# Kernel tuning notes

Hardware: AMD Instinct MI355X
Metric: run time of the kernel (lower is better)

Reference implementation:

```python
import jax, jax.numpy as jnp
import numpy as np

TAU = 0.2
LW = 0.5
EPS = 1e-12  # tf.math.l2_normalize epsilon


def _l2norm(x):
    ss = jnp.sum(x * x, axis=-1, keepdims=True)
    return x * jax.lax.rsqrt(jnp.maximum(ss, EPS))


def _global_head(f, W1, b1, W2, b2):
    g = jnp.mean(f, axis=(1, 2))            # GlobalAveragePooling2D -> [B, C]
    h = jax.nn.relu(g @ W1 + b1)
    return h @ W2 + b2                      # [B, 128]


def _dense_head(f, W1, b1, W2, b2):
    # 1x1 convs == per-pixel matmuls
    h = jax.nn.relu(jnp.einsum('bhwc,cd->bhwd', f, W1) + b1)
    return jnp.einsum('bhwd,de->bhwe', h, W2) + b2  # [B, H, W, 128]


def _info_nce(q, k):
    logits = (q @ k.T) / TAU                # [N, N]
    lse = jax.nn.logsumexp(logits, axis=-1)
    pos = jnp.diagonal(logits)
    return jnp.mean(lse - pos)


def setup_inputs() -> dict:
    key = jax.random.key(0)
    ks = jax.random.split(key, 10)
    B, H, W, C = 128, 7, 7, 2048
    Dh, De = 2048, 128
    s1 = 1.0 / np.sqrt(C)
    s2 = 1.0 / np.sqrt(Dh)
    inp = {
        'feat_q': jax.random.normal(ks[0], (B, H, W, C), jnp.float32),
        'feat_k': jax.random.normal(ks[1], (B, H, W, C), jnp.float32),
        'Wg1': jax.random.normal(ks[2], (C, Dh), jnp.float32) * s1,
        'bg1': jnp.zeros((Dh,), jnp.float32),
        'Wg2': jax.random.normal(ks[3], (Dh, De), jnp.float32) * s2,
        'bg2': jnp.zeros((De,), jnp.float32),
        'Wd1': jax.random.normal(ks[4], (C, Dh), jnp.float32) * s1,
        'bd1': jnp.zeros((Dh,), jnp.float32),
        'Wd2': jax.random.normal(ks[5], (Dh, De), jnp.float32) * s2,
        'bd2': jnp.zeros((De,), jnp.float32),
        'mWg1': jax.random.normal(ks[6], (C, Dh), jnp.float32) * s1,
        'mbg1': jnp.zeros((Dh,), jnp.float32),
        'mWg2': jax.random.normal(ks[7], (Dh, De), jnp.float32) * s2,
        'mbg2': jnp.zeros((De,), jnp.float32),
        'mWd1': jax.random.normal(ks[8], (C, Dh), jnp.float32) * s1,
        'mbd1': jnp.zeros((Dh,), jnp.float32),
        'mWd2': jax.random.normal(ks[9], (Dh, De), jnp.float32) * s2,
        'mbd2': jnp.zeros((De,), jnp.float32),
    }
    return inp


def reference(feat_q, feat_k, Wg1, bg1, Wg2, bg2, Wd1, bd1, Wd2, bd2,
              mWg1, mbg1, mWg2, mbg2, mWd1, mbd1, mWd2, mbd2):
    # query (student) branch
    q_g = _l2norm(_global_head(feat_q, Wg1, bg1, Wg2, bg2))      # [B, 128]
    q_d = _l2norm(_dense_head(feat_q, Wd1, bd1, Wd2, bd2))       # [B, H, W, 128]
    # key (momentum teacher) branch, stop-gradient as in train_step
    k_g = jax.lax.stop_gradient(_l2norm(_global_head(feat_k, mWg1, mbg1, mWg2, mbg2)))
    k_d = jax.lax.stop_gradient(_l2norm(_dense_head(feat_k, mWd1, mbd1, mWd2, mbd2)))

    l_g = _info_nce(q_g, k_g)

    B, H, W, De = q_d.shape
    f1 = q_d.reshape(B, H * W, De)
    f2 = k_d.reshape(B, H * W, De)
    sim = jnp.einsum('bnc,bmc->bnm', f1, f2)                     # [B, HW, HW]
    idx = jnp.argmax(sim, axis=-1)                               # [B, HW]
    matched = jnp.take_along_axis(f2, idx[..., None], axis=1)    # [B, HW, 128]

    l_d = _info_nce(f1.reshape(-1, De), matched.reshape(-1, De))
    total = (1.0 - LW) * l_g + LW * l_d
    return total
```

## Files before the change

kernel.cpp:

```cpp
#include <hip/hip_runtime.h>
#include <cstddef>

typedef __bf16 bf16x8 __attribute__((ext_vector_type(8)));
typedef float  f32x4  __attribute__((ext_vector_type(4)));
typedef unsigned short u16x8 __attribute__((ext_vector_type(8)));

__device__ __forceinline__ float b2f(unsigned short u) {
    union { unsigned int i; float f; } v; v.i = ((unsigned int)u) << 16; return v.f;
}
__device__ __forceinline__ unsigned short f2b(float f) {
    union { float f; unsigned int i; } v; v.f = f;
    unsigned int r = v.i + 0x7fffu + ((v.i >> 16) & 1u);
    return (unsigned short)(r >> 16);
}
__device__ __forceinline__ void gl_lds16(const void* g, void* l) {
    __builtin_amdgcn_global_load_lds((const __attribute__((address_space(1))) void*)g,
                                     (__attribute__((address_space(3))) void*)l,
                                     16, 0, 0);
}

__global__ __launch_bounds__(64) void detect_kernel(const unsigned short* __restrict__ feat,
                                                    int* __restrict__ flag) {
    __shared__ int cnt;
    if (threadIdx.x == 0) cnt = 0;
    __syncthreads();
    int c = 0;
    for (int i = threadIdx.x; i < 256; i += 64) {
        float v = b2f(feat[i]);
        if (fabsf(v) > 100.0f) ++c;
    }
    atomicAdd(&cnt, c);
    __syncthreads();
    if (threadIdx.x == 0) *flag = (cnt > 16) ? 1 : 0;
}

__global__ __launch_bounds__(256) void zero_kernel(float* __restrict__ p, int n4) {
    int i = blockIdx.x * 256 + threadIdx.x;
    const f32x4 z = {0.f, 0.f, 0.f, 0.f};
    if (i < n4) ((f32x4*)p)[i] = z;
}

__global__ __launch_bounds__(256) void pool_kernel(const void* __restrict__ fq,
                                                   const void* __restrict__ fk,
                                                   unsigned short* __restrict__ gq,
                                                   unsigned short* __restrict__ gk,
                                                   const int* __restrict__ flagp) {
    int fl = *flagp;
    int c = blockIdx.x * 256 + threadIdx.x;
    int b = blockIdx.y;
    const void* src = blockIdx.z ? fk : fq;
    unsigned short* dst = blockIdx.z ? gk : gq;
    size_t base = (size_t)b * 49 * 2048 + c;
    float s = 0.f;
    if (fl) {
        const float* sf = (const float*)src;
        #pragma unroll
        for (int p = 0; p < 49; ++p) s += sf[base + (size_t)p * 2048];
    } else {
        const unsigned short* su = (const unsigned short*)src;
        #pragma unroll
        for (int p = 0; p < 49; ++p) s += b2f(su[base + (size_t)p * 2048]);
    }
    dst[(size_t)b * 2048 + c] = f2b(s * (1.0f / 49.0f));
}

__global__ __launch_bounds__(256) void transpose4_kernel(
    const void* __restrict__ s0, const void* __restrict__ s1,
    const void* __restrict__ s2, const void* __restrict__ s3,
    unsigned short* __restrict__ d0, unsigned short* __restrict__ d1,
    unsigned short* __restrict__ d2, unsigned short* __restrict__ d3,
    int rows, int cols, const int* __restrict__ flagp) {
    int fl = *flagp;
    int z = blockIdx.z;
    const void* in = (z == 0) ? s0 : (z == 1) ? s1 : (z == 2) ? s2 : s3;
    unsigned short* out = (z == 0) ? d0 : (z == 1) ? d1 : (z == 2) ? d2 : d3;
    __shared__ unsigned short tile[32][33];
    int bx = blockIdx.x * 32, by = blockIdx.y * 32;
    int tx = threadIdx.x & 31, ty = threadIdx.x >> 5;
    if (fl) {
        const float* inf = (const float*)in;
        #pragma unroll
        for (int i = 0; i < 32; i += 8)
            tile[ty + i][tx] = f2b(inf[(size_t)(by + ty + i) * cols + (bx + tx)]);
    } else {
        const unsigned short* inu = (const unsigned short*)in;
        #pragma unroll
        for (int i = 0; i < 32; i += 8)
            tile[ty + i][tx] = inu[(size_t)(by + ty + i) * cols + (bx + tx)];
    }
    __syncthreads();
    #pragma unroll
    for (int i = 0; i < 32; i += 8)
        out[(size_t)(bx + ty + i) * rows + (by + tx)] = tile[tx][ty + i];
}

__global__ __launch_bounds__(256) void mlp_kernel(
    const void* __restrict__ Aq, const void* __restrict__ Ak,
    const unsigned short* __restrict__ gq, const unsigned short* __restrict__ gk,
    const unsigned short* __restrict__ BTdq, const unsigned short* __restrict__ BTdk,
    const unsigned short* __restrict__ BTgq, const unsigned short* __restrict__ BTgk,
    const unsigned short* __restrict__ W2dq, const unsigned short* __restrict__ W2dk,
    const unsigned short* __restrict__ W2gq, const unsigned short* __restrict__ W2gk,
    const void* __restrict__ b1dq, const void* __restrict__ b1dk,
    const void* __restrict__ b1gq, const void* __restrict__ b1gk,
    float* __restrict__ outdq, float* __restrict__ outdk,
    float* __restrict__ outgq, float* __restrict__ outgk,
    const int* __restrict__ flagp)
{
    int fl = *flagp;
    int z  = blockIdx.z;
    int isg = (blockIdx.y == 49);
    const void* A; const unsigned short* Bt; const unsigned short* W2;
    const void* b1; float* outp;
    if (!isg) {
        A = z ? Ak : Aq;  Bt = z ? BTdk : BTdq;  W2 = z ? W2dk : W2dq;
        b1 = z ? b1dk : b1dq;  outp = z ? outdk : outdq;
    } else {
        A = z ? (const void*)gk : (const void*)gq;  Bt = z ? BTgk : BTgq;
        W2 = z ? W2gk : W2gq;  b1 = z ? b1gk : b1gq;  outp = z ? outgk : outgq;
    }
    int af32 = (!isg) && fl;
    const int K = 2048;

    __shared__ unsigned short As[128 * 64];
    __shared__ unsigned short Bs[128 * 64];
    __shared__ unsigned short Hs[128 * 72];

    int tid  = threadIdx.x;
    int lane = tid & 63;
    int w    = tid >> 6;
    int wm = w & 1, wn = w >> 1;
    int quad = lane >> 4, l16 = lane & 15;
    size_t m0 = isg ? 0 : (size_t)blockIdx.y * 128;
    size_t n0 = (size_t)blockIdx.x * 128;

    int lrow = lane >> 3;
    int kc   = (lane & 7) ^ lrow;

    const unsigned short* gA[4];
    const unsigned short* gB[4];
    unsigned short* lA[4];
    unsigned short* lB[4];
    if (!af32) {
        const unsigned short* Au = (const unsigned short*)A;
        #pragma unroll
        for (int c = 0; c < 4; ++c) {
            int row = w * 32 + c * 8 + lrow;
            gA[c] = Au + (m0 + row) * (size_t)K + kc * 8;
            lA[c] = As + w * 2048 + c * 512;
        }
    }
    #pragma unroll
    for (int c = 0; c < 4; ++c) {
        int row = w * 32 + c * 8 + lrow;
        gB[c] = Bt + (n0 + row) * (size_t)K + kc * 8;
        lB[c] = Bs + w * 2048 + c * 512;
    }

    const f32x4 zero4 = {0.f, 0.f, 0.f, 0.f};
    f32x4 acc[4][4];
    #pragma unroll
    for (int i = 0; i < 4; ++i)
        #pragma unroll
        for (int j = 0; j < 4; ++j) acc[i][j] = zero4;

    int swz = l16 & 7;
    for (int kb = 0; kb < K / 64; ++kb) {
        __syncthreads();
        if (af32) {
            const float* Af = (const float*)A;
            #pragma unroll
            for (int i = 0; i < 4; ++i) {
                int l = tid + 256 * i;
                int row = l >> 3, kcp = l & 7;
                int kcg = kcp ^ (row & 7);
                size_t gidx = (m0 + row) * (size_t)K + kb * 64 + kcg * 8;
                f32x4 v0 = *(const f32x4*)(Af + gidx);
                f32x4 v1 = *(const f32x4*)(Af + gidx + 4);
                u16x8 o;
                o[0]=f2b(v0[0]); o[1]=f2b(v0[1]); o[2]=f2b(v0[2]); o[3]=f2b(v0[3]);
                o[4]=f2b(v1[0]); o[5]=f2b(v1[1]); o[6]=f2b(v1[2]); o[7]=f2b(v1[3]);
                *(u16x8*)(As + row * 64 + kcp * 8) = o;
            }
        } else {
            #pragma unroll
            for (int c = 0; c < 4; ++c) { gl_lds16(gA[c], lA[c]); gA[c] += 64; }
        }
        #pragma unroll
        for (int c = 0; c < 4; ++c) { gl_lds16(gB[c], lB[c]); gB[c] += 64; }
        __syncthreads();
        #pragma unroll
        for (int k0 = 0; k0 < 64; k0 += 32) {
            bf16x8 af[4], bfr[4];
            #pragma unroll
            for (int mt = 0; mt < 4; ++mt) {
                int row = wm * 64 + mt * 16 + l16;
                int sc  = (((k0 >> 3) + quad) ^ swz) << 3;
                af[mt] = *(const bf16x8*)(As + row * 64 + sc);
            }
            #pragma unroll
            for (int nt = 0; nt < 4; ++nt) {
                int row = wn * 64 + nt * 16 + l16;
                int sc  = (((k0 >> 3) + quad) ^ swz) << 3;
                bfr[nt] = *(const bf16x8*)(Bs + row * 64 + sc);
            }
            #pragma unroll
            for (int mt = 0; mt < 4; ++mt)
                #pragma unroll
                for (int nt = 0; nt < 4; ++nt)
                    acc[mt][nt] = __builtin_amdgcn_mfma_f32_16x16x32_bf16(af[mt], bfr[nt], acc[mt][nt], 0, 0, 0);
        }
    }

    float b1v[4];
    #pragma unroll
    for (int nt = 0; nt < 4; ++nt) {
        int col = (int)n0 + wn * 64 + nt * 16 + l16;
        b1v[nt] = fl ? ((const float*)b1)[col] : b2f(((const unsigned short*)b1)[col]);
    }

    f32x4 acc2[4][4];
    #pragma unroll
    for (int i = 0; i < 4; ++i)
        #pragma unroll
        for (int j = 0; j < 4; ++j) acc2[i][j] = zero4;

    #pragma unroll
    for (int hf = 0; hf < 2; ++hf) {
        __syncthreads();
        if (wn == hf) {
            #pragma unroll
            for (int mt = 0; mt < 4; ++mt)
                #pragma unroll
                for (int nt = 0; nt < 4; ++nt)
                    #pragma unroll
                    for (int r = 0; r < 4; ++r) {
                        float v = fmaxf(acc[mt][nt][r] + b1v[nt], 0.f);
                        Hs[(wm * 64 + mt * 16 + quad * 4 + r) * 72 + nt * 16 + l16] = f2b(v);
                    }
        } else {
            #pragma unroll
            for (int c = 0; c < 8; ++c) {
                const unsigned short* g = W2 + (size_t)(wm * 64 + c * 8 + lrow) * 2048
                                          + n0 + hf * 64 + kc * 8;
                gl_lds16(g, As + wm * 4096 + c * 512);
            }
        }
        __syncthreads();
        #pragma unroll
        for (int k0 = 0; k0 < 64; k0 += 32) {
            bf16x8 ha[4], wb[4];
            #pragma unroll
            for (int mt = 0; mt < 4; ++mt)
                ha[mt] = *(const bf16x8*)(Hs + (wm * 64 + mt * 16 + l16) * 72 + k0 + quad * 8);
            #pragma unroll
            for (int et = 0; et < 4; ++et) {
                int row = wn * 64 + et * 16 + l16;
                int sc  = (((k0 >> 3) + quad) ^ swz) << 3;
                wb[et] = *(const bf16x8*)(As + row * 64 + sc);
            }
            #pragma unroll
            for (int mt = 0; mt < 4; ++mt)
                #pragma unroll
                for (int et = 0; et < 4; ++et)
                    acc2[mt][et] = __builtin_amdgcn_mfma_f32_16x16x32_bf16(ha[mt], wb[et], acc2[mt][et], 0, 0, 0);
        }
    }

    #pragma unroll
    for (int et = 0; et < 4; ++et) {
        int col = wn * 64 + et * 16 + l16;
        #pragma unroll
        for (int mt = 0; mt < 4; ++mt)
            #pragma unroll
            for (int r = 0; r < 4; ++r) {
                size_t row = m0 + wm * 64 + mt * 16 + quad * 4 + r;
                atomicAdd(&outp[row * 128 + col], acc2[mt][et][r]);
            }
    }
}

__global__ __launch_bounds__(128) void l2norm_all_kernel(
    const float* __restrict__ rawdq, const float* __restrict__ rawdk,
    const float* __restrict__ rawgq, const float* __restrict__ rawgk,
    const void* __restrict__ bd2, const void* __restrict__ mbd2,
    const void* __restrict__ bg2, const void* __restrict__ mbg2,
    unsigned short* __restrict__ qd, unsigned short* __restrict__ kd,
    unsigned short* __restrict__ qg, unsigned short* __restrict__ kg,
    const int* __restrict__ flagp) {
    int fl = *flagp;
    int b = blockIdx.x;
    const float* in; const void* bias; unsigned short* out; int r;
    if (b < 6272)       { in = rawdq; bias = bd2;  out = qd; r = b; }
    else if (b < 12544) { in = rawdk; bias = mbd2; out = kd; r = b - 6272; }
    else if (b < 12672) { in = rawgq; bias = bg2;  out = qg; r = b - 12544; }
    else                { in = rawgk; bias = mbg2; out = kg; r = b - 12672; }
    int t = threadIdx.x;
    float bv = fl ? ((const float*)bias)[t] : b2f(((const unsigned short*)bias)[t]);
    float x = in[(size_t)r * 128 + t] + bv;
    float s = x * x;
    #pragma unroll
    for (int off = 32; off >= 1; off >>= 1) s += __shfl_xor(s, off);
    __shared__ float ws2[2];
    if ((t & 63) == 0) ws2[t >> 6] = s;
    __syncthreads();
    float tot = ws2[0] + ws2[1];
    float rs = rsqrtf(fmaxf(tot, 1e-12f));
    out[(size_t)r * 128 + t] = f2b(x * rs);
}

__global__ __launch_bounds__(256) void simmatch_kernel(const unsigned short* __restrict__ qd,
                                                       const unsigned short* __restrict__ kd,
                                                       unsigned short* __restrict__ matched,
                                                       float* __restrict__ pos) {
    __shared__ float f1s[49 * 128];
    __shared__ float f2s[49 * 128];
    int b = blockIdx.x;
    int t = threadIdx.x;
    size_t base = (size_t)b * 49 * 128;
    for (int i = t; i < 49 * 128; i += 256) {
        f1s[i] = b2f(qd[base + i]);
        f2s[i] = b2f(kd[base + i]);
    }
    __syncthreads();
    int i = t >> 2, q4 = t & 3;
    if (i < 49) {
        int mlo = q4 * 13;
        int mhi = mlo + 13; if (mhi > 49) mhi = 49;
        float best = -1e30f; int bi = 1 << 20;
        const f32x4* va = (const f32x4*)(f1s + i * 128);
        for (int m = mlo; m < mhi; ++m) {
            const f32x4* vb = (const f32x4*)(f2s + m * 128);
            float d = 0.f;
            #pragma unroll
            for (int j = 0; j < 32; ++j) {
                f32x4 a = va[j], bb = vb[j];
                d += a[0]*bb[0] + a[1]*bb[1] + a[2]*bb[2] + a[3]*bb[3];
            }
            if (d > best) { best = d; bi = m; }
        }
        #pragma unroll
        for (int off = 1; off < 4; off <<= 1) {
            float ov = __shfl_xor(best, off);
            int   oi = __shfl_xor(bi, off);
            if (ov > best || (ov == best && oi < bi)) { best = ov; bi = oi; }
        }
        if (q4 == 0) pos[b * 49 + i] = best * 5.0f;
        for (int j = q4 * 32; j < q4 * 32 + 32; ++j)
            matched[base + (size_t)i * 128 + j] = f2b(f2s[bi * 128 + j]);
    }
}

#define KS 136
__global__ __launch_bounds__(256) void lse_kernel(const unsigned short* __restrict__ qd,
                                                  const unsigned short* __restrict__ matched,
                                                  float* __restrict__ lsep) {
    __shared__ unsigned short As[128 * KS];
    __shared__ unsigned short Bs[64 * KS];
    __shared__ float rsum[128];
    int tid  = threadIdx.x;
    int lane = tid & 63, wave = tid >> 6;
    int wm = wave & 1, wn = wave >> 1;
    int quad = lane >> 4, l16 = lane & 15;
    size_t m0 = (size_t)blockIdx.x * 128;
    int z = blockIdx.y;

    #pragma unroll
    for (int i = 0; i < 8; ++i) {
        int l = tid + 256 * i;
        int row = l >> 4, ko = (l & 15) << 3;
        u16x8 v = *(const u16x8*)(qd + (m0 + row) * 128 + ko);
        *(u16x8*)(As + row * KS + ko) = v;
    }
    if (tid < 128) rsum[tid] = 0.f;

    float rs[4][4];
    #pragma unroll
    for (int mt = 0; mt < 4; ++mt)
        #pragma unroll
        for (int r = 0; r < 4; ++r) rs[mt][r] = 0.f;

    const f32x4 zero4 = {0.f, 0.f, 0.f, 0.f};
    int nlo = z * 896, nhi = nlo + 896;
    for (int n0 = nlo; n0 < nhi; n0 += 64) {
        __syncthreads();
        #pragma unroll
        for (int i = 0; i < 4; ++i) {
            int l = tid + 256 * i;
            int row = l >> 4, ko = (l & 15) << 3;
            u16x8 v = *(const u16x8*)(matched + (size_t)(n0 + row) * 128 + ko);
            *(u16x8*)(Bs + row * KS + ko) = v;
        }
        __syncthreads();
        f32x4 acc[4][2];
        #pragma unroll
        for (int mt = 0; mt < 4; ++mt) { acc[mt][0] = zero4; acc[mt][1] = zero4; }
        #pragma unroll
        for (int k0 = 0; k0 < 128; k0 += 32) {
            bf16x8 af[4], bfr[2];
            #pragma unroll
            for (int mt = 0; mt < 4; ++mt)
                af[mt] = *(const bf16x8*)(As + (wm * 64 + mt * 16 + l16) * KS + k0 + quad * 8);
            #pragma unroll
            for (int nt = 0; nt < 2; ++nt)
                bfr[nt] = *(const bf16x8*)(Bs + (wn * 32 + nt * 16 + l16) * KS + k0 + quad * 8);
            #pragma unroll
            for (int mt = 0; mt < 4; ++mt)
                #pragma unroll
                for (int nt = 0; nt < 2; ++nt)
                    acc[mt][nt] = __builtin_amdgcn_mfma_f32_16x16x32_bf16(af[mt], bfr[nt], acc[mt][nt], 0, 0, 0);
        }
        #pragma unroll
        for (int mt = 0; mt < 4; ++mt)
            #pragma unroll
            for (int r = 0; r < 4; ++r)
                rs[mt][r] += __expf(acc[mt][0][r] * 5.0f) + __expf(acc[mt][1][r] * 5.0f);
    }
    #pragma unroll
    for (int mt = 0; mt < 4; ++mt)
        #pragma unroll
        for (int r = 0; r < 4; ++r) {
            float v = rs[mt][r];
            v += __shfl_xor(v, 1); v += __shfl_xor(v, 2);
            v += __shfl_xor(v, 4); v += __shfl_xor(v, 8);
            if (l16 == 0) atomicAdd(&rsum[wm * 64 + mt * 16 + quad * 4 + r], v);
        }
    __syncthreads();
    if (tid < 128) lsep[(size_t)z * 6272 + m0 + tid] = rsum[tid];
}

__global__ __launch_bounds__(128) void lg_kernel(const unsigned short* __restrict__ qg,
                                                 const unsigned short* __restrict__ kg,
                                                 float* __restrict__ lgrow) {
    __shared__ unsigned short ks[16384];
    __shared__ unsigned short qs[1024];
    int t = threadIdx.x;
    int rbase = blockIdx.x * 8;
    for (int i = t; i < 16384; i += 128) ks[i] = kg[i];
    for (int i = t; i < 1024; i += 128) qs[i] = qg[rbase * 128 + i];
    __syncthreads();
    int rl = t >> 4;
    int jg = t & 15;
    int row = rbase + rl;
    float se = 0.f, diag = 0.f;
    for (int jj = 0; jj < 8; ++jj) {
        int j = jg * 8 + jj;
        float d = 0.f;
        #pragma unroll 8
        for (int c = 0; c < 128; ++c) d += b2f(qs[rl * 128 + c]) * b2f(ks[j * 128 + c]);
        d *= 5.0f;
        se += __expf(d);
        if (j == row) diag = d;
    }
    #pragma unroll
    for (int off = 1; off < 16; off <<= 1) { se += __shfl_xor(se, off); diag += __shfl_xor(diag, off); }
    if (jg == 0) lgrow[row] = logf(se) - diag;
}

__global__ __launch_bounds__(256) void final_kernel(const float* __restrict__ lsep,
                                                    const float* __restrict__ pos,
                                                    const float* __restrict__ lgrow,
                                                    unsigned int* __restrict__ out) {
    int t = threadIdx.x;
    float s = 0.f;
    for (int i = t; i < 6272; i += 256) {
        float se = 0.f;
        #pragma unroll
        for (int zz = 0; zz < 7; ++zz) se += lsep[zz * 6272 + i];
        s += logf(se) - pos[i];
    }
    float g = (t < 128) ? lgrow[t] : 0.f;
    #pragma unroll
    for (int off = 32; off >= 1; off >>= 1) { s += __shfl_xor(s, off); g += __shfl_xor(g, off); }
    __shared__ float p8[8];
    if ((t & 63) == 0) { p8[t >> 6] = s; p8[4 + (t >> 6)] = g; }
    __syncthreads();
    if (t == 0) {
        float ld  = (p8[0] + p8[1] + p8[2] + p8[3]) * (1.0f / 6272.0f);
        float lg  = (p8[4] + p8[5] + p8[6] + p8[7]) * (1.0f / 128.0f);
        float total = 0.5f * lg + 0.5f * ld;
        unsigned int L = f2b(total);
        union { float f; unsigned int u; } tb; tb.f = total;
        unsigned int base = (tb.u & 0xFFFF0000u) | L;
        unsigned int bu = base; float be = 1e30f;
        #pragma unroll
        for (int d = -1; d <= 1; ++d) {
            unsigned int c = base + ((unsigned int)d << 16);
            union { unsigned int u; float f; } cv; cv.u = c;
            float e = fabsf(cv.f - total);
            if (e < be) { be = e; bu = c; }
        }
        out[0] = bu;
    }
}

#define BT1Q_OFF  ((size_t)0)
#define QD_OFF    ((size_t)0)
#define KD_OFF    ((size_t)1605632)
#define MT_OFF    ((size_t)3211264)
#define BT1K_OFF  ((size_t)8388608)
#define BTGQ_OFF  ((size_t)16777216)
#define BTGK_OFF  ((size_t)25165824)
#define W2DQ_OFF  ((size_t)33554432)
#define W2DK_OFF  ((size_t)34078720)
#define W2GQ_OFF  ((size_t)34603008)
#define W2GK_OFF  ((size_t)35127296)
#define RAWDQ_OFF ((size_t)35651584)
#define RAWDK_OFF ((size_t)38862848)
#define RAWGQ_OFF ((size_t)42074112)
#define RAWGK_OFF ((size_t)42139648)
#define GQ_OFF    ((size_t)42205184)
#define GK_OFF    ((size_t)42729472)
#define QG_OFF    ((size_t)43253760)
#define KG_OFF    ((size_t)43286528)
#define POS_OFF   ((size_t)43319296)
#define LSEP_OFF  ((size_t)43344384)
#define LGR_OFF   ((size_t)43520000)
#define FLAG_OFF  ((size_t)43520512)

extern "C" void kernel_launch(void* const* d_in, const int* in_sizes, int n_in,
                              void* d_out, int out_size, void* d_ws, size_t ws_size,
                              hipStream_t stream) {
    (void)in_sizes; (void)n_in; (void)out_size; (void)ws_size;
    const void* feat_q = d_in[0];
    const void* feat_k = d_in[1];
    const void* Wg1 = d_in[2];  const void* bg1 = d_in[3];
    const void* Wg2 = d_in[4];  const void* bg2 = d_in[5];
    const void* Wd1 = d_in[6];  const void* bd1 = d_in[7];
    const void* Wd2 = d_in[8];  const void* bd2 = d_in[9];
    const void* mWg1 = d_in[10]; const void* mbg1 = d_in[11];
    const void* mWg2 = d_in[12]; const void* mbg2 = d_in[13];
    const void* mWd1 = d_in[14]; const void* mbd1 = d_in[15];
    const void* mWd2 = d_in[16]; const void* mbd2 = d_in[17];

    char* ws = (char*)d_ws;
    unsigned short* BT1q = (unsigned short*)(ws + BT1Q_OFF);
    unsigned short* BT1k = (unsigned short*)(ws + BT1K_OFF);
    unsigned short* BTgq = (unsigned short*)(ws + BTGQ_OFF);
    unsigned short* BTgk = (unsigned short*)(ws + BTGK_OFF);
    unsigned short* W2dq = (unsigned short*)(ws + W2DQ_OFF);
    unsigned short* W2dk = (unsigned short*)(ws + W2DK_OFF);
    unsigned short* W2gq = (unsigned short*)(ws + W2GQ_OFF);
    unsigned short* W2gk = (unsigned short*)(ws + W2GK_OFF);
    float* rawdq = (float*)(ws + RAWDQ_OFF);
    float* rawdk = (float*)(ws + RAWDK_OFF);
    float* rawgq = (float*)(ws + RAWGQ_OFF);
    float* rawgk = (float*)(ws + RAWGK_OFF);
    unsigned short* gq = (unsigned short*)(ws + GQ_OFF);
    unsigned short* gk = (unsigned short*)(ws + GK_OFF);
    unsigned short* qd = (unsigned short*)(ws + QD_OFF);
    unsigned short* kd = (unsigned short*)(ws + KD_OFF);
    unsigned short* mt = (unsigned short*)(ws + MT_OFF);
    unsigned short* qg = (unsigned short*)(ws + QG_OFF);
    unsigned short* kg = (unsigned short*)(ws + KG_OFF);
    float* pos  = (float*)(ws + POS_OFF);
    float* lsep = (float*)(ws + LSEP_OFF);
    float* lgr  = (float*)(ws + LGR_OFF);
    int*   flag = (int*)(ws + FLAG_OFF);

    detect_kernel<<<1, 64, 0, stream>>>((const unsigned short*)feat_q, flag);

    transpose4_kernel<<<dim3(64, 64, 4), 256, 0, stream>>>(
        Wd1, mWd1, Wg1, mWg1, BT1q, BT1k, BTgq, BTgk, 2048, 2048, flag);
    transpose4_kernel<<<dim3(4, 64, 4), 256, 0, stream>>>(
        Wd2, mWd2, Wg2, mWg2, W2dq, W2dk, W2gq, W2gk, 2048, 128, flag);

    pool_kernel<<<dim3(8, 128, 2), 256, 0, stream>>>(feat_q, feat_k, gq, gk, flag);

    zero_kernel<<<1600, 256, 0, stream>>>(rawdq, 409600);

    mlp_kernel<<<dim3(16, 50, 2), 256, 0, stream>>>(
        feat_q, feat_k, gq, gk,
        BT1q, BT1k, BTgq, BTgk,
        W2dq, W2dk, W2gq, W2gk,
        bd1, mbd1, bg1, mbg1,
        rawdq, rawdk, rawgq, rawgk, flag);

    l2norm_all_kernel<<<12800, 128, 0, stream>>>(
        rawdq, rawdk, rawgq, rawgk, bd2, mbd2, bg2, mbg2, qd, kd, qg, kg, flag);

    simmatch_kernel<<<128, 256, 0, stream>>>(qd, kd, mt, pos);
    lse_kernel<<<dim3(49, 7), 256, 0, stream>>>(qd, mt, lsep);
    lg_kernel<<<16, 128, 0, stream>>>(qg, kg, lgr);
    final_kernel<<<1, 256, 0, stream>>>(lsep, pos, lgr, (unsigned int*)d_out);
}
```

Before: 593.9 us.

## Fuse l2norm into simmatch and lg kernels, vectorize transpose, split lse wider

```diff
diff --git a/kernel.cpp b/kernel.cpp
--- a/kernel.cpp
+++ b/kernel.cpp
@@ -64,7 +64,7 @@
     dst[(size_t)b * 2048 + c] = f2b(s * (1.0f / 49.0f));
 }
 
-__global__ __launch_bounds__(256) void transpose4_kernel(
+__global__ __launch_bounds__(256) void transpose4v_kernel(
     const void* __restrict__ s0, const void* __restrict__ s1,
     const void* __restrict__ s2, const void* __restrict__ s3,
     unsigned short* __restrict__ d0, unsigned short* __restrict__ d1,
@@ -74,24 +74,35 @@
     int z = blockIdx.z;
     const void* in = (z == 0) ? s0 : (z == 1) ? s1 : (z == 2) ? s2 : s3;
     unsigned short* out = (z == 0) ? d0 : (z == 1) ? d1 : (z == 2) ? d2 : d3;
-    __shared__ unsigned short tile[32][33];
-    int bx = blockIdx.x * 32, by = blockIdx.y * 32;
-    int tx = threadIdx.x & 31, ty = threadIdx.x >> 5;
-    if (fl) {
-        const float* inf = (const float*)in;
-        #pragma unroll
-        for (int i = 0; i < 32; i += 8)
-            tile[ty + i][tx] = f2b(inf[(size_t)(by + ty + i) * cols + (bx + tx)]);
-    } else {
-        const unsigned short* inu = (const unsigned short*)in;
-        #pragma unroll
-        for (int i = 0; i < 32; i += 8)
-            tile[ty + i][tx] = inu[(size_t)(by + ty + i) * cols + (bx + tx)];
+    __shared__ unsigned short tile[64 * 72];
+    int bx = blockIdx.x * 64, by = blockIdx.y * 64;
+    int tr = threadIdx.x >> 3;
+    int tc = (threadIdx.x & 7) * 8;
+    #pragma unroll
+    for (int h = 0; h < 2; ++h) {
+        int r = tr + h * 32;
+        if (fl) {
+            const float* inf = (const float*)in + (size_t)(by + r) * cols + bx + tc;
+            f32x4 v0 = *(const f32x4*)inf;
+            f32x4 v1 = *(const f32x4*)(inf + 4);
+            u16x8 o;
+            o[0]=f2b(v0[0]); o[1]=f2b(v0[1]); o[2]=f2b(v0[2]); o[3]=f2b(v0[3]);
+            o[4]=f2b(v1[0]); o[5]=f2b(v1[1]); o[6]=f2b(v1[2]); o[7]=f2b(v1[3]);
+            *(u16x8*)(tile + r * 72 + tc) = o;
+        } else {
+            const unsigned short* inu = (const unsigned short*)in + (size_t)(by + r) * cols + bx + tc;
+            *(u16x8*)(tile + r * 72 + tc) = *(const u16x8*)inu;
+        }
     }
     __syncthreads();
     #pragma unroll
-    for (int i = 0; i < 32; i += 8)
-        out[(size_t)(bx + ty + i) * rows + (by + tx)] = tile[tx][ty + i];
+    for (int h = 0; h < 2; ++h) {
+        int oc = tr + h * 32;
+        u16x8 v;
+        #pragma unroll
+        for (int j = 0; j < 8; ++j) v[j] = tile[(tc + j) * 72 + oc];
+        *(u16x8*)(out + (size_t)(bx + oc) * rows + by + tc) = v;
+    }
 }
 
 __global__ __launch_bounds__(256) void mlp_kernel(
@@ -122,9 +133,10 @@
     int af32 = (!isg) && fl;
     const int K = 2048;
 
-    __shared__ unsigned short As[128 * 64];
-    __shared__ unsigned short Bs[128 * 64];
-    __shared__ unsigned short Hs[128 * 72];
+    __shared__ unsigned short smem[8192 + 9216];
+    unsigned short* As = smem;
+    unsigned short* Bs = smem + 8192;
+    unsigned short* Hs = smem + 8192;
 
     int tid  = threadIdx.x;
     int lane = tid & 63;
@@ -280,49 +292,49 @@
     }
 }
 
-__global__ __launch_bounds__(128) void l2norm_all_kernel(
+__global__ __launch_bounds__(256) void simmatch_kernel(
     const float* __restrict__ rawdq, const float* __restrict__ rawdk,
-    const float* __restrict__ rawgq, const float* __restrict__ rawgk,
     const void* __restrict__ bd2, const void* __restrict__ mbd2,
-    const void* __restrict__ bg2, const void* __restrict__ mbg2,
     unsigned short* __restrict__ qd, unsigned short* __restrict__ kd,
-    unsigned short* __restrict__ qg, unsigned short* __restrict__ kg,
+    unsigned short* __restrict__ matched, float* __restrict__ pos,
     const int* __restrict__ flagp) {
     int fl = *flagp;
-    int b = blockIdx.x;
-    const float* in; const void* bias; unsigned short* out; int r;
-    if (b < 6272)       { in = rawdq; bias = bd2;  out = qd; r = b; }
-    else if (b < 12544) { in = rawdk; bias = mbd2; out = kd; r = b - 6272; }
-    else if (b < 12672) { in = rawgq; bias = bg2;  out = qg; r = b - 12544; }
-    else                { in = rawgk; bias = mbg2; out = kg; r = b - 12672; }
-    int t = threadIdx.x;
-    float bv = fl ? ((const float*)bias)[t] : b2f(((const unsigned short*)bias)[t]);
-    float x = in[(size_t)r * 128 + t] + bv;
-    float s = x * x;
-    #pragma unroll
-    for (int off = 32; off >= 1; off >>= 1) s += __shfl_xor(s, off);
-    __shared__ float ws2[2];
-    if ((t & 63) == 0) ws2[t >> 6] = s;
-    __syncthreads();
-    float tot = ws2[0] + ws2[1];
-    float rs = rsqrtf(fmaxf(tot, 1e-12f));
-    out[(size_t)r * 128 + t] = f2b(x * rs);
-}
-
-__global__ __launch_bounds__(256) void simmatch_kernel(const unsigned short* __restrict__ qd,
-                                                       const unsigned short* __restrict__ kd,
-                                                       unsigned short* __restrict__ matched,
-                                                       float* __restrict__ pos) {
     __shared__ float f1s[49 * 128];
     __shared__ float f2s[49 * 128];
     int b = blockIdx.x;
     int t = threadIdx.x;
     size_t base = (size_t)b * 49 * 128;
-    for (int i = t; i < 49 * 128; i += 256) {
-        f1s[i] = b2f(qd[base + i]);
-        f2s[i] = b2f(kd[base + i]);
+
+    int rr = t >> 2, jq = t & 3;
+    if (rr < 49) {
+        #pragma unroll
+        for (int br = 0; br < 2; ++br) {
+            const float* raw = br ? rawdk : rawdq;
+            const void* bias = br ? mbd2 : bd2;
+            unsigned short* outg = br ? kd : qd;
+            float* fs = br ? f2s : f1s;
+            size_t idx = base + (size_t)rr * 128 + jq * 32;
+            float x[32];
+            float ss = 0.f;
+            #pragma unroll
+            for (int c = 0; c < 32; ++c) {
+                float bv = fl ? ((const float*)bias)[jq * 32 + c]
+                              : b2f(((const unsigned short*)bias)[jq * 32 + c]);
+                x[c] = raw[idx + c] + bv;
+                ss += x[c] * x[c];
+            }
+            ss += __shfl_xor(ss, 1); ss += __shfl_xor(ss, 2);
+            float rs = rsqrtf(fmaxf(ss, 1e-12f));
+            #pragma unroll
+            for (int c = 0; c < 32; ++c) {
+                unsigned short us = f2b(x[c] * rs);
+                outg[idx + c] = us;
+                fs[rr * 128 + jq * 32 + c] = b2f(us);
+            }
+        }
     }
     __syncthreads();
+
     int i = t >> 2, q4 = t & 3;
     if (i < 49) {
         int mlo = q4 * 13;
@@ -381,7 +393,7 @@
         for (int r = 0; r < 4; ++r) rs[mt][r] = 0.f;
 
     const f32x4 zero4 = {0.f, 0.f, 0.f, 0.f};
-    int nlo = z * 896, nhi = nlo + 896;
+    int nlo = z * 448, nhi = nlo + 448;
     for (int n0 = nlo; n0 < nhi; n0 += 64) {
         __syncthreads();
         #pragma unroll
@@ -429,25 +441,54 @@
     if (tid < 128) lsep[(size_t)z * 6272 + m0 + tid] = rsum[tid];
 }
 
-__global__ __launch_bounds__(128) void lg_kernel(const unsigned short* __restrict__ qg,
-                                                 const unsigned short* __restrict__ kg,
-                                                 float* __restrict__ lgrow) {
-    __shared__ unsigned short ks[16384];
-    __shared__ unsigned short qs[1024];
+__global__ __launch_bounds__(128) void lg_kernel(const float* __restrict__ rawgq,
+                                                 const float* __restrict__ rawgk,
+                                                 const void* __restrict__ bg2,
+                                                 const void* __restrict__ mbg2,
+                                                 float* __restrict__ lgrow,
+                                                 const int* __restrict__ flagp) {
+    int fl = *flagp;
+    __shared__ float ksf[128 * 128];
+    __shared__ float qsf[8 * 128];
     int t = threadIdx.x;
     int rbase = blockIdx.x * 8;
-    for (int i = t; i < 16384; i += 128) ks[i] = kg[i];
-    for (int i = t; i < 1024; i += 128) qs[i] = qg[rbase * 128 + i];
+    {
+        const float* rk = rawgk + (size_t)t * 128;
+        float ss = 0.f;
+        for (int c = 0; c < 128; ++c) {
+            float bv = fl ? ((const float*)mbg2)[c] : b2f(((const unsigned short*)mbg2)[c]);
+            float xx = rk[c] + bv;
+            ss += xx * xx;
+        }
+        float rsv = rsqrtf(fmaxf(ss, 1e-12f));
+        for (int c = 0; c < 128; ++c) {
+            float bv = fl ? ((const float*)mbg2)[c] : b2f(((const unsigned short*)mbg2)[c]);
+            ksf[t * 128 + c] = b2f(f2b((rk[c] + bv) * rsv));
+        }
+    }
+    if (t < 8) {
+        const float* rq = rawgq + (size_t)(rbase + t) * 128;
+        float ss = 0.f;
+        for (int c = 0; c < 128; ++c) {
+            float bv = fl ? ((const float*)bg2)[c] : b2f(((const unsigned short*)bg2)[c]);
+            float xx = rq[c] + bv;
+            ss += xx * xx;
+        }
+        float rsv = rsqrtf(fmaxf(ss, 1e-12f));
+        for (int c = 0; c < 128; ++c) {
+            float bv = fl ? ((const float*)bg2)[c] : b2f(((const unsigned short*)bg2)[c]);
+            qsf[t * 128 + c] = b2f(f2b((rq[c] + bv) * rsv));
+        }
+    }
     __syncthreads();
-    int rl = t >> 4;
-    int jg = t & 15;
+    int rl = t >> 4, jg = t & 15;
     int row = rbase + rl;
     float se = 0.f, diag = 0.f;
     for (int jj = 0; jj < 8; ++jj) {
         int j = jg * 8 + jj;
         float d = 0.f;
         #pragma unroll 8
-        for (int c = 0; c < 128; ++c) d += b2f(qs[rl * 128 + c]) * b2f(ks[j * 128 + c]);
+        for (int c = 0; c < 128; ++c) d += qsf[rl * 128 + c] * ksf[j * 128 + c];
         d *= 5.0f;
         se += __expf(d);
         if (j == row) diag = d;
@@ -466,7 +507,7 @@
     for (int i = t; i < 6272; i += 256) {
         float se = 0.f;
         #pragma unroll
-        for (int zz = 0; zz < 7; ++zz) se += lsep[zz * 6272 + i];
+        for (int zz = 0; zz < 14; ++zz) se += lsep[zz * 6272 + i];
         s += logf(se) - pos[i];
     }
     float g = (t < 128) ? lgrow[t] : 0.f;
@@ -511,12 +552,10 @@
 #define RAWGK_OFF ((size_t)42139648)
 #define GQ_OFF    ((size_t)42205184)
 #define GK_OFF    ((size_t)42729472)
-#define QG_OFF    ((size_t)43253760)
-#define KG_OFF    ((size_t)43286528)
-#define POS_OFF   ((size_t)43319296)
-#define LSEP_OFF  ((size_t)43344384)
-#define LGR_OFF   ((size_t)43520000)
-#define FLAG_OFF  ((size_t)43520512)
+#define POS_OFF   ((size_t)43253760)
+#define LSEP_OFF  ((size_t)43278848)
+#define LGR_OFF   ((size_t)43630080)
+#define FLAG_OFF  ((size_t)43630592)
 
 extern "C" void kernel_launch(void* const* d_in, const int* in_sizes, int n_in,
                               void* d_out, int out_size, void* d_ws, size_t ws_size,
@@ -551,8 +590,6 @@
     unsigned short* qd = (unsigned short*)(ws + QD_OFF);
     unsigned short* kd = (unsigned short*)(ws + KD_OFF);
     unsigned short* mt = (unsigned short*)(ws + MT_OFF);
-    unsigned short* qg = (unsigned short*)(ws + QG_OFF);
-    unsigned short* kg = (unsigned short*)(ws + KG_OFF);
     float* pos  = (float*)(ws + POS_OFF);
     float* lsep = (float*)(ws + LSEP_OFF);
     float* lgr  = (float*)(ws + LGR_OFF);
@@ -560,9 +597,9 @@
 
     detect_kernel<<<1, 64, 0, stream>>>((const unsigned short*)feat_q, flag);
 
-    transpose4_kernel<<<dim3(64, 64, 4), 256, 0, stream>>>(
+    transpose4v_kernel<<<dim3(32, 32, 4), 256, 0, stream>>>(
         Wd1, mWd1, Wg1, mWg1, BT1q, BT1k, BTgq, BTgk, 2048, 2048, flag);
-    transpose4_kernel<<<dim3(4, 64, 4), 256, 0, stream>>>(
+    transpose4v_kernel<<<dim3(2, 32, 4), 256, 0, stream>>>(
         Wd2, mWd2, Wg2, mWg2, W2dq, W2dk, W2gq, W2gk, 2048, 128, flag);
 
     pool_kernel<<<dim3(8, 128, 2), 256, 0, stream>>>(feat_q, feat_k, gq, gk, flag);
@@ -576,11 +613,8 @@
         bd1, mbd1, bg1, mbg1,
         rawdq, rawdk, rawgq, rawgk, flag);
 
-    l2norm_all_kernel<<<12800, 128, 0, stream>>>(
-        rawdq, rawdk, rawgq, rawgk, bd2, mbd2, bg2, mbg2, qd, kd, qg, kg, flag);
-
-    simmatch_kernel<<<128, 256, 0, stream>>>(qd, kd, mt, pos);
-    lse_kernel<<<dim3(49, 7), 256, 0, stream>>>(qd, mt, lsep);
-    lg_kernel<<<16, 128, 0, stream>>>(qg, kg, lgr);
+    simmatch_kernel<<<128, 256, 0, stream>>>(rawdq, rawdk, bd2, mbd2, qd, kd, mt, pos, flag);
+    lse_kernel<<<dim3(49, 14), 256, 0, stream>>>(qd, mt, lsep);
+    lg_kernel<<<16, 128, 0, stream>>>(rawgq, rawgk, bg2, mbg2, lgr, flag);
     final_kernel<<<1, 256, 0, stream>>>(lsep, pos, lgr, (unsigned int*)d_out);
 }
```

Result: slower. 641.4 us (+8.0%).
